# Optimization experiments

Hardware: AMD Instinct MI355X
Metric: run time of the kernel (lower is better)

## Reference

```python
import jax, jax.numpy as jnp
import numpy as np

N = 16      # num_blocks (grid is N x N)
D = 256     # block_size (homogeneous)
B = 2048    # batch_size
ITERS = 3   # num_iterations
# Static block-sparsity: block (i, j) exists iff j <= i + 1 (banded lower grid).
MASK = np.array([[1.0 if j <= i + 1 else 0.0 for j in range(N)] for i in range(N)], dtype=np.float32)


def setup_inputs() -> dict:
    key = jax.random.key(0)
    k1, k2, k3 = jax.random.split(key, 3)
    x0 = jax.random.normal(k1, (B, D), dtype=jnp.float32)
    # W[i, j] is the (out=D, in=D) weight of the Linear mapping block j -> block i.
    W = jax.random.normal(k2, (N, N, D, D), dtype=jnp.float32) * (1.0 / np.sqrt(D))
    b = jax.random.normal(k3, (N, N, D), dtype=jnp.float32) * 0.01
    return {"x0": x0, "W": W, "b": b}


def reference(x0, W, b):
    mask = jnp.asarray(MASK)
    Wm = W * mask[:, :, None, None]   # zero out absent grid blocks
    bm = b * mask[:, :, None]
    # Iteration 1: format_input pads with None, so only input block j=0 exists;
    # row i output = blocks[i][0](x0) (bias of block (i,0) only).
    Y = jnp.einsum('bd,med->mbe', x0, Wm[:, 0]) + bm[:, 0][:, None, :]   # [N, B, D]
    Y = jax.nn.relu(Y)
    # Remaining iterations: all N block inputs are present.
    bias_full = jnp.sum(bm, axis=1)   # [N, D] sum of biases over present blocks per row
    for _ in range(ITERS - 1):
        Y = jnp.einsum('nbd,mned->mbe', Y, Wm) + bias_full[:, None, :]
        Y = jax.nn.relu(Y)
    return Y  # [N, B, D]
```

## Files before the change

### kernel.cpp

```cpp
#include <hip/hip_runtime.h>
#include <hip/hip_bf16.h>
#include <stdint.h>


#define DD    256
#define NBLK  16
#define BATCH 2048

typedef __attribute__((ext_vector_type(8))) short  bf16x8;
typedef __attribute__((ext_vector_type(8))) __bf16 bfv8;
typedef __attribute__((ext_vector_type(4))) float  f32x4;

__device__ __forceinline__ unsigned short f2bf(float f) {
  return __builtin_bit_cast(unsigned short, (__bf16)f);
}

__device__ __forceinline__ void gload_lds16(const unsigned short* g, unsigned short* l) {
  __builtin_amdgcn_global_load_lds((const __attribute__((address_space(1))) void*)g,
                                   (__attribute__((address_space(3))) void*)l, 16, 0, 0);
}

__device__ __forceinline__ bf16x8 cvt8(float4 lo, float4 hi) {
  bfv8 t;
  t[0] = (__bf16)lo.x; t[1] = (__bf16)lo.y; t[2] = (__bf16)lo.z; t[3] = (__bf16)lo.w;
  t[4] = (__bf16)hi.x; t[5] = (__bf16)hi.y; t[6] = (__bf16)hi.z; t[7] = (__bf16)hi.w;
  return __builtin_bit_cast(bf16x8, t);
}


__global__ void cvt_x0_kernel(const float* __restrict__ x, unsigned short* __restrict__ y) {
  int i = blockIdx.x * 256 + threadIdx.x;
  float4 v = ((const float4*)x)[i];
  ushort4 o;
  o.x = f2bf(v.x); o.y = f2bf(v.y); o.z = f2bf(v.z); o.w = f2bf(v.w);
  ((ushort4*)y)[i] = o;
}

__global__ void bias_full_kernel(const float* __restrict__ b, float* __restrict__ bf) {
  int idx = blockIdx.x * 256 + threadIdx.x;
  int m = idx >> 8, e = idx & 255;
  int nb = (m + 2 < NBLK) ? m + 2 : NBLK;
  float s = 0.f;
  for (int j = 0; j < nb; ++j) s += b[(m * NBLK + j) * DD + e];
  bf[idx] = s;
}


template <int OUT_BF16>
__global__ __launch_bounds__(256, 2) void gemm_step(
    const unsigned short* __restrict__ A,
    const float* __restrict__ Wg,
    const float* __restrict__ bias,
    int bias_stride,
    long a_nstride,
    int nb_mode,
    void* __restrict__ Out)
{
  __shared__ unsigned short ldsA[2][128 * 64];
  __shared__ unsigned short ldsW[2][128 * 64];

  const int tid  = threadIdx.x;
  const int wave = tid >> 6;
  const int lane = tid & 63;

  int bid = blockIdx.x;
  int swz = (bid & 7) * 64 + (bid >> 3);
  int mi_ = swz >> 5;
  const int m = (int)((0x8796A5B4C3D2E1F0ULL >> (mi_ * 4)) & 15);
  int rest = swz & 31;
  const int btile = rest >> 1;
  const int etile = rest & 1;
  const int nb = nb_mode ? ((m + 2 < NBLK) ? m + 2 : NBLK) : 1;
  const int nt = nb << 2;

  const int brow0 = btile * 128;
  const int ecol0 = etile * 128;
  const int wr = (wave >> 1) & 1;
  const int wc = wave & 1;

  long a_goff[4];
  int  a_lds[4];
#pragma unroll
  for (int i = 0; i < 4; ++i) {
    int inst  = wave * 4 + i;
    int row   = inst * 8 + (lane >> 3);
    int chunk = (lane & 7) ^ (row & 7);
    a_goff[i] = (long)(brow0 + row) * DD + chunk * 8;
    a_lds[i]  = inst * 512;
  }

  long w_goff[4];
  int  w_lds[4];
#pragma unroll
  for (int u = 0; u < 4; ++u) {
    int cid = tid + 256 * u;
    int row = cid >> 3;
    int c16 = cid & 7;
    w_goff[u] = (long)(ecol0 + row) * DD + c16 * 8;
    w_lds[u]  = row * 64 + ((c16 ^ (row & 7)) * 8);
  }

  int offA[4][2], offW[4][2];
#pragma unroll
  for (int f = 0; f < 4; ++f) {
    int ra = wr * 64 + f * 16 + (lane & 15);
    int rw = wc * 64 + f * 16 + (lane & 15);
#pragma unroll
    for (int ks = 0; ks < 2; ++ks) {
      int byteoff = ks * 64 + (lane >> 4) * 16;
      offA[f][ks] = ra * 64 + (((byteoff ^ ((ra & 7) << 4))) >> 1);
      offW[f][ks] = rw * 64 + (((byteoff ^ ((rw & 7) << 4))) >> 1);
    }
  }

  f32x4 acc[4][4];
#pragma unroll
  for (int i = 0; i < 4; ++i)
#pragma unroll
    for (int j = 0; j < 4; ++j) acc[i][j] = (f32x4){0.f, 0.f, 0.f, 0.f};

  const long wm_base = (long)m * NBLK * (DD * DD);

  {
#pragma unroll
    for (int i = 0; i < 4; ++i)
      gload_lds16(A + a_goff[i], &ldsA[0][a_lds[i]]);
    const float* Wn = Wg + wm_base;
#pragma unroll
    for (int u = 0; u < 4; ++u) {
      float4 lo = *(const float4*)(Wn + w_goff[u]);
      float4 hi = *(const float4*)(Wn + w_goff[u] + 4);
      *(bf16x8*)&ldsW[0][w_lds[u]] = cvt8(lo, hi);
    }
  }
  __syncthreads();

  int cur = 0;
  for (int t = 0; t < nt; ++t) {
    const int nxt = cur ^ 1;
    const bool has_next = (t + 1 < nt);
    float4 wlo[4], whi[4];
    if (has_next) {
      int n2  = (t + 1) >> 2;
      int kk2 = ((t + 1) & 3) * 64;
      const unsigned short* An = A + (long)n2 * a_nstride + kk2;
#pragma unroll
      for (int i = 0; i < 4; ++i)
        gload_lds16(An + a_goff[i], &ldsA[nxt][a_lds[i]]);
      const float* Wn = Wg + wm_base + (long)n2 * (DD * DD) + kk2;
#pragma unroll
      for (int u = 0; u < 4; ++u) {
        wlo[u] = *(const float4*)(Wn + w_goff[u]);
        whi[u] = *(const float4*)(Wn + w_goff[u] + 4);
      }
    }
#pragma unroll
    for (int ks = 0; ks < 2; ++ks) {
      bf16x8 af[4], wf[4];
#pragma unroll
      for (int f = 0; f < 4; ++f) af[f] = *(const bf16x8*)&ldsA[cur][offA[f][ks]];
#pragma unroll
      for (int f = 0; f < 4; ++f) wf[f] = *(const bf16x8*)&ldsW[cur][offW[f][ks]];
#pragma unroll
      for (int i = 0; i < 4; ++i)
#pragma unroll
        for (int j = 0; j < 4; ++j)
          acc[i][j] = __builtin_amdgcn_mfma_f32_16x16x32_bf16(af[i], wf[j], acc[i][j], 0, 0, 0);
    }
    if (has_next) {
#pragma unroll
      for (int u = 0; u < 4; ++u)
        *(bf16x8*)&ldsW[nxt][w_lds[u]] = cvt8(wlo[u], whi[u]);
    }
    __syncthreads();
    cur = nxt;
  }

  const long outbase = (long)m * BATCH * DD;
  const int  rowbase = brow0 + wr * 64;
  const int  colbase = ecol0 + wc * 64;
#pragma unroll
  for (int j = 0; j < 4; ++j) {
    const int col = colbase + j * 16 + (lane & 15);
    const float bv = bias[m * bias_stride + col];
#pragma unroll
    for (int i = 0; i < 4; ++i) {
      const int row0 = rowbase + i * 16 + ((lane >> 4) << 2);
#pragma unroll
      for (int r = 0; r < 4; ++r) {
        float v = acc[i][j][r] + bv;
        v = v > 0.f ? v : 0.f;
        long idx = outbase + (long)(row0 + r) * DD + col;
        if (OUT_BF16) ((unsigned short*)Out)[idx] = f2bf(v);
        else          ((float*)Out)[idx] = v;
      }
    }
  }
}


extern "C" void kernel_launch(void* const* d_in, const int* in_sizes, int n_in,
                              void* d_out, int out_size, void* d_ws, size_t ws_size,
                              hipStream_t stream) {
  const float* x0 = (const float*)d_in[0];
  const float* W  = (const float*)d_in[1];
  const float* b  = (const float*)d_in[2];
  float* out = (float*)d_out;

  char* ws = (char*)d_ws;
  unsigned short* x0b  = (unsigned short*)ws;
  unsigned short* Y0   = (unsigned short*)(ws + (1ull << 20));
  unsigned short* Y1   = (unsigned short*)(ws + (17ull << 20));
  float* bias_full     = (float*)(ws + (33ull << 20));

  cvt_x0_kernel<<<512, 256, 0, stream>>>(x0, x0b);
  bias_full_kernel<<<16, 256, 0, stream>>>(b, bias_full);

  gemm_step<1><<<512, 256, 0, stream>>>(x0b, W, b, NBLK * DD, 0L, 0, (void*)Y0);
  gemm_step<1><<<512, 256, 0, stream>>>(Y0, W, bias_full, DD, (long)BATCH * DD, 1, (void*)Y1);
  gemm_step<0><<<512, 256, 0, stream>>>(Y1, W, bias_full, DD, (long)BATCH * DD, 1, (void*)out);
}
```

Before: 311.8 us.

## Pre-convert present W blocks to packed bf16 and stream via direct LDS loads

New measurement: 251.8 us. 19.2% less time.

```diff
diff --git a/kernel.cpp b/kernel.cpp
--- a/kernel.cpp
+++ b/kernel.cpp
@@ -10,6 +10,8 @@
 typedef __attribute__((ext_vector_type(8))) short  bf16x8;
 typedef __attribute__((ext_vector_type(8))) __bf16 bfv8;
 typedef __attribute__((ext_vector_type(4))) float  f32x4;
+
+__device__ __constant__ int Pofs[17] = {0,2,5,9,14,20,27,35,44,54,65,77,90,104,119,135,151};
 
 __device__ __forceinline__ unsigned short f2bf(float f) {
   return __builtin_bit_cast(unsigned short, (__bf16)f);
@@ -45,11 +47,24 @@
   bf[idx] = s;
 }
 
+__global__ void cvt_W_kernel(const float* __restrict__ W, unsigned short* __restrict__ Wb) {
+  int p = blockIdx.x >> 5;
+  int m = 0;
+#pragma unroll
+  for (int k = 1; k <= 15; ++k) if (p >= Pofs[k]) m = k;
+  int n = p - Pofs[m];
+  long idx = (long)(blockIdx.x & 31) * 2048 + threadIdx.x * 8;
+  const float* src = W + (long)(m * NBLK + n) * (DD * DD) + idx;
+  float4 lo = *(const float4*)src;
+  float4 hi = *(const float4*)(src + 4);
+  *(bf16x8*)(Wb + (long)p * (DD * DD) + idx) = cvt8(lo, hi);
+}
+
 
 template <int OUT_BF16>
-__global__ __launch_bounds__(256, 2) void gemm_step(
+__global__ __launch_bounds__(256, 2) void gemm_step2(
     const unsigned short* __restrict__ A,
-    const float* __restrict__ Wg,
+    const unsigned short* __restrict__ Wb,
     const float* __restrict__ bias,
     int bias_stride,
     long a_nstride,
@@ -78,8 +93,128 @@
   const int wr = (wave >> 1) & 1;
   const int wc = wave & 1;
 
-  long a_goff[4];
-  int  a_lds[4];
+  long a_goff[4], w_goff[4];
+  int  s_lds[4];
+#pragma unroll
+  for (int i = 0; i < 4; ++i) {
+    int inst  = wave * 4 + i;
+    int row   = inst * 8 + (lane >> 3);
+    int chunk = (lane & 7) ^ (row & 7);
+    a_goff[i] = (long)(brow0 + row) * DD + chunk * 8;
+    w_goff[i] = (long)(ecol0 + row) * DD + chunk * 8;
+    s_lds[i]  = inst * 512;
+  }
+
+  int offA[4][2], offW[4][2];
+#pragma unroll
+  for (int f = 0; f < 4; ++f) {
+    int ra = wr * 64 + f * 16 + (lane & 15);
+    int rw = wc * 64 + f * 16 + (lane & 15);
+#pragma unroll
+    for (int ks = 0; ks < 2; ++ks) {
+      int byteoff = ks * 64 + (lane >> 4) * 16;
+      offA[f][ks] = ra * 64 + ((byteoff ^ ((ra & 7) << 4)) >> 1);
+      offW[f][ks] = rw * 64 + ((byteoff ^ ((rw & 7) << 4)) >> 1);
+    }
+  }
+
+  f32x4 acc[4][4];
+#pragma unroll
+  for (int i = 0; i < 4; ++i)
+#pragma unroll
+    for (int j = 0; j < 4; ++j) acc[i][j] = (f32x4){0.f, 0.f, 0.f, 0.f};
+
+  const unsigned short* Wrow = Wb + (long)Pofs[m] * (DD * DD);
+
+#pragma unroll
+  for (int i = 0; i < 4; ++i) {
+    gload_lds16(A + a_goff[i],    &ldsA[0][s_lds[i]]);
+    gload_lds16(Wrow + w_goff[i], &ldsW[0][s_lds[i]]);
+  }
+  __syncthreads();
+
+  int cur = 0;
+  for (int t = 0; t < nt; ++t) {
+    const int nxt = cur ^ 1;
+    if (t + 1 < nt) {
+      int n2  = (t + 1) >> 2;
+      int kk2 = ((t + 1) & 3) * 64;
+      const unsigned short* An = A + (long)n2 * a_nstride + kk2;
+      const unsigned short* Wn = Wrow + (long)n2 * (DD * DD) + kk2;
+#pragma unroll
+      for (int i = 0; i < 4; ++i) {
+        gload_lds16(An + a_goff[i], &ldsA[nxt][s_lds[i]]);
+        gload_lds16(Wn + w_goff[i], &ldsW[nxt][s_lds[i]]);
+      }
+    }
+#pragma unroll
+    for (int ks = 0; ks < 2; ++ks) {
+      bf16x8 af[4], wf[4];
+#pragma unroll
+      for (int f = 0; f < 4; ++f) af[f] = *(const bf16x8*)&ldsA[cur][offA[f][ks]];
+#pragma unroll
+      for (int f = 0; f < 4; ++f) wf[f] = *(const bf16x8*)&ldsW[cur][offW[f][ks]];
+#pragma unroll
+      for (int i = 0; i < 4; ++i)
+#pragma unroll
+        for (int j = 0; j < 4; ++j)
+          acc[i][j] = __builtin_amdgcn_mfma_f32_16x16x32_bf16(af[i], wf[j], acc[i][j], 0, 0, 0);
+    }
+    __syncthreads();
+    cur = nxt;
+  }
+
+  const long outbase = (long)m * BATCH * DD;
+  const int  rowbase = brow0 + wr * 64;
+  const int  colbase = ecol0 + wc * 64;
+#pragma unroll
+  for (int j = 0; j < 4; ++j) {
+    const int col = colbase + j * 16 + (lane & 15);
+    const float bv = bias[m * bias_stride + col];
+#pragma unroll
+    for (int i = 0; i < 4; ++i) {
+      const int row0 = rowbase + i * 16 + ((lane >> 4) << 2);
+#pragma unroll
+      for (int r = 0; r < 4; ++r) {
+        float v = acc[i][j][r] + bv;
+        v = v > 0.f ? v : 0.f;
+        long idx = outbase + (long)(row0 + r) * DD + col;
+        if (OUT_BF16) ((unsigned short*)Out)[idx] = f2bf(v);
+        else          ((float*)Out)[idx] = v;
+      }
+    }
+  }
+}
+
+
+template <int OUT_BF16>
+__global__ __launch_bounds__(256, 2) void gemm_step(
+    const unsigned short* __restrict__ A,
+    const float* __restrict__ Wg,
+    const float* __restrict__ bias,
+    int bias_stride, long a_nstride, int nb_mode,
+    void* __restrict__ Out)
+{
+  __shared__ unsigned short ldsA[2][128 * 64];
+  __shared__ unsigned short ldsW[2][128 * 64];
+  const int tid  = threadIdx.x;
+  const int wave = tid >> 6;
+  const int lane = tid & 63;
+  int bid = blockIdx.x;
+  int swz = (bid & 7) * 64 + (bid >> 3);
+  int mi_ = swz >> 5;
+  const int m = (int)((0x8796A5B4C3D2E1F0ULL >> (mi_ * 4)) & 15);
+  int rest = swz & 31;
+  const int btile = rest >> 1;
+  const int etile = rest & 1;
+  const int nb = nb_mode ? ((m + 2 < NBLK) ? m + 2 : NBLK) : 1;
+  const int nt = nb << 2;
+  const int brow0 = btile * 128;
+  const int ecol0 = etile * 128;
+  const int wr = (wave >> 1) & 1;
+  const int wc = wave & 1;
+
+  long a_goff[4]; int a_lds[4];
 #pragma unroll
   for (int i = 0; i < 4; ++i) {
     int inst  = wave * 4 + i;
@@ -88,9 +223,7 @@
     a_goff[i] = (long)(brow0 + row) * DD + chunk * 8;
     a_lds[i]  = inst * 512;
   }
-
-  long w_goff[4];
-  int  w_lds[4];
+  long w_goff[4]; int w_lds[4];
 #pragma unroll
   for (int u = 0; u < 4; ++u) {
     int cid = tid + 256 * u;
@@ -99,7 +232,6 @@
     w_goff[u] = (long)(ecol0 + row) * DD + c16 * 8;
     w_lds[u]  = row * 64 + ((c16 ^ (row & 7)) * 8);
   }
-
   int offA[4][2], offW[4][2];
 #pragma unroll
   for (int f = 0; f < 4; ++f) {
@@ -108,23 +240,19 @@
 #pragma unroll
     for (int ks = 0; ks < 2; ++ks) {
       int byteoff = ks * 64 + (lane >> 4) * 16;
-      offA[f][ks] = ra * 64 + (((byteoff ^ ((ra & 7) << 4))) >> 1);
-      offW[f][ks] = rw * 64 + (((byteoff ^ ((rw & 7) << 4))) >> 1);
-    }
-  }
-
+      offA[f][ks] = ra * 64 + ((byteoff ^ ((ra & 7) << 4)) >> 1);
+      offW[f][ks] = rw * 64 + ((byteoff ^ ((rw & 7) << 4)) >> 1);
+    }
+  }
   f32x4 acc[4][4];
 #pragma unroll
   for (int i = 0; i < 4; ++i)
 #pragma unroll
-    for (int j = 0; j < 4; ++j) acc[i][j] = (f32x4){0.f, 0.f, 0.f, 0.f};
-
+    for (int j = 0; j < 4; ++j) acc[i][j] = (f32x4){0.f,0.f,0.f,0.f};
   const long wm_base = (long)m * NBLK * (DD * DD);
-
   {
 #pragma unroll
-    for (int i = 0; i < 4; ++i)
-      gload_lds16(A + a_goff[i], &ldsA[0][a_lds[i]]);
+    for (int i = 0; i < 4; ++i) gload_lds16(A + a_goff[i], &ldsA[0][a_lds[i]]);
     const float* Wn = Wg + wm_base;
 #pragma unroll
     for (int u = 0; u < 4; ++u) {
@@ -134,7 +262,6 @@
     }
   }
   __syncthreads();
-
   int cur = 0;
   for (int t = 0; t < nt; ++t) {
     const int nxt = cur ^ 1;
@@ -145,8 +272,7 @@
       int kk2 = ((t + 1) & 3) * 64;
       const unsigned short* An = A + (long)n2 * a_nstride + kk2;
 #pragma unroll
-      for (int i = 0; i < 4; ++i)
-        gload_lds16(An + a_goff[i], &ldsA[nxt][a_lds[i]]);
+      for (int i = 0; i < 4; ++i) gload_lds16(An + a_goff[i], &ldsA[nxt][a_lds[i]]);
       const float* Wn = Wg + wm_base + (long)n2 * (DD * DD) + kk2;
 #pragma unroll
       for (int u = 0; u < 4; ++u) {
@@ -175,7 +301,6 @@
     __syncthreads();
     cur = nxt;
   }
-
   const long outbase = (long)m * BATCH * DD;
   const int  rowbase = brow0 + wr * 64;
   const int  colbase = ecol0 + wc * 64;
@@ -208,15 +333,28 @@
   float* out = (float*)d_out;
 
   char* ws = (char*)d_ws;
-  unsigned short* x0b  = (unsigned short*)ws;
-  unsigned short* Y0   = (unsigned short*)(ws + (1ull << 20));
-  unsigned short* Y1   = (unsigned short*)(ws + (17ull << 20));
-  float* bias_full     = (float*)(ws + (33ull << 20));
+  unsigned short* x0b = (unsigned short*)ws;
+  unsigned short* Y0  = (unsigned short*)(ws + (1ull << 20));
+  unsigned short* Y1  = (unsigned short*)(ws + (17ull << 20));
+
+  const size_t wb_bytes = 151ull * DD * DD * 2;
+  const size_t need = (33ull << 20) + wb_bytes + 16384;
 
   cvt_x0_kernel<<<512, 256, 0, stream>>>(x0, x0b);
-  bias_full_kernel<<<16, 256, 0, stream>>>(b, bias_full);
-
-  gemm_step<1><<<512, 256, 0, stream>>>(x0b, W, b, NBLK * DD, 0L, 0, (void*)Y0);
-  gemm_step<1><<<512, 256, 0, stream>>>(Y0, W, bias_full, DD, (long)BATCH * DD, 1, (void*)Y1);
-  gemm_step<0><<<512, 256, 0, stream>>>(Y1, W, bias_full, DD, (long)BATCH * DD, 1, (void*)out);
-}
+
+  if (ws_size >= need) {
+    unsigned short* Wb = (unsigned short*)(ws + (33ull << 20));
+    float* bias_full   = (float*)(ws + (33ull << 20) + wb_bytes);
+    bias_full_kernel<<<16, 256, 0, stream>>>(b, bias_full);
+    cvt_W_kernel<<<151 * 32, 256, 0, stream>>>(W, Wb);
+    gemm_step2<1><<<512, 256, 0, stream>>>(x0b, Wb, b, NBLK * DD, 0L, 0, (void*)Y0);
+    gemm_step2<1><<<512, 256, 0, stream>>>(Y0, Wb, bias_full, DD, (long)BATCH * DD, 1, (void*)Y1);
+    gemm_step2<0><<<512, 256, 0, stream>>>(Y1, Wb, bias_full, DD, (long)BATCH * DD, 1, (void*)out);
+  } else {
+    float* bias_full = (float*)(ws + (33ull << 20));
+    bias_full_kernel<<<16, 256, 0, stream>>>(b, bias_full);
+    gemm_step<1><<<512, 256, 0, stream>>>(x0b, W, b, NBLK * DD, 0L, 0, (void*)Y0);
+    gemm_step<1><<<512, 256, 0, stream>>>(Y0, W, bias_full, DD, (long)BATCH * DD, 1, (void*)Y1);
+    gemm_step<0><<<512, 256, 0, stream>>>(Y1, W, bias_full, DD, (long)BATCH * DD, 1, (void*)out);
+  }
+}
```
